# Optimization experiments

Measured on AMD Instinct MI355X. Metric: run time of the kernel, lower is better.

## Reference

```python
import jax, jax.numpy as jnp
import numpy as np
from jax import lax

NBINS = 256


def setup_inputs() -> dict:
    key = jax.random.key(0)
    y_pred = jax.random.uniform(key, (64, 3, 512, 512), dtype=jnp.float32)
    return {"y_pred": y_pred}


def reference(y_pred):
    # Faithful to: per-batch torch.histc(bins=256) (range = data min/max),
    # normalize to probs, entropy in bits with 0*log2(0)=0, mean over batch.
    B = y_pred.shape[0]
    x = y_pred.reshape(B, -1)  # [B, N]
    mn = jnp.min(x, axis=1, keepdims=True)
    mx = jnp.max(x, axis=1, keepdims=True)
    # torch.histc: if min == max they are adjusted to min-1 / max+1
    rng = jnp.where(mx > mn, mx - mn, 2.0)
    lo = jnp.where(mx > mn, mn, mn - 1.0)
    idx = jnp.clip(((x - lo) * (NBINS / rng)).astype(jnp.int32), 0, NBINS - 1)
    idx = lax.stop_gradient(idx)  # binning is non-differentiable (as in torch.histc)
    hist = jax.vmap(lambda i: jnp.bincount(i, length=NBINS))(idx)  # [B, 256]
    hist = hist.astype(y_pred.dtype)
    p = hist / jnp.sum(hist, axis=1, keepdims=True)
    safe_p = jnp.where(p == 0, 1.0, p)  # log2(1)=0 -> contributes 0
    ent = -jnp.sum(p * jnp.log2(safe_p), axis=1)  # [B], entropy in bits
    return jnp.mean(ent)
```

## Files before the change

kernel.cpp:

```cpp
#include <hip/hip_runtime.h>

#define NBINS   256
#define B       64
#define NPB     786432
#define NF4     (NPB / 4)
#define BPB1    32
#define BPB2    16
#define THREADS 256

__global__ __launch_bounds__(THREADS) void k_minmax(const float4* __restrict__ x,
                                                    float* __restrict__ pmn,
                                                    float* __restrict__ pmx) {
    const int batch = blockIdx.x / BPB1;
    const int blk   = blockIdx.x % BPB1;
    const float4* p = x + (long long)batch * NF4;

    float mn = 3.402823466e38f, mx = -3.402823466e38f;
    #pragma unroll 4
    for (int i = blk * THREADS + threadIdx.x; i < NF4; i += BPB1 * THREADS) {
        float4 v = p[i];
        mn = fminf(mn, fminf(fminf(v.x, v.y), fminf(v.z, v.w)));
        mx = fmaxf(mx, fmaxf(fmaxf(v.x, v.y), fmaxf(v.z, v.w)));
    }
    for (int o = 32; o > 0; o >>= 1) {
        mn = fminf(mn, __shfl_down(mn, o));
        mx = fmaxf(mx, __shfl_down(mx, o));
    }
    __shared__ float smn[4], smx[4];
    int wid = threadIdx.x >> 6;
    if ((threadIdx.x & 63) == 0) { smn[wid] = mn; smx[wid] = mx; }
    __syncthreads();
    if (threadIdx.x == 0) {
        pmn[blockIdx.x] = fminf(fminf(smn[0], smn[1]), fminf(smn[2], smn[3]));
        pmx[blockIdx.x] = fmaxf(fmaxf(smx[0], smx[1]), fmaxf(smx[2], smx[3]));
    }
}

__global__ __launch_bounds__(THREADS) void k_hist(const float4* __restrict__ x,
                                                  const float* __restrict__ pmn,
                                                  const float* __restrict__ pmx,
                                                  unsigned* __restrict__ part) {
    __shared__ unsigned lh[NBINS * 32];
    __shared__ float s_lo, s_scale;

    const int batch = blockIdx.x / BPB2;
    const int blk   = blockIdx.x % BPB2;

    for (int i = threadIdx.x; i < NBINS * 32; i += THREADS) lh[i] = 0u;

    if (threadIdx.x < 64) {
        int l = threadIdx.x & 31;
        float mn = pmn[batch * BPB1 + l];
        float mx = pmx[batch * BPB1 + l];
        for (int o = 16; o > 0; o >>= 1) {
            mn = fminf(mn, __shfl_down(mn, o));
            mx = fmaxf(mx, __shfl_down(mx, o));
        }
        if (threadIdx.x == 0) {
            float rng = (mx > mn) ? (mx - mn) : 2.0f;
            s_lo      = (mx > mn) ? mn : (mn - 1.0f);
            s_scale   = (float)NBINS / rng;
        }
    }
    __syncthreads();

    const float lo    = s_lo;
    const float scale = s_scale;
    const int   g     = threadIdx.x & 31;
    const float4* p   = x + (long long)batch * NF4;

    #pragma unroll 2
    for (int i = blk * THREADS + threadIdx.x; i < NF4; i += BPB2 * THREADS) {
        float4 v = p[i];
        int i0 = min(max((int)((v.x - lo) * scale), 0), NBINS - 1);
        int i1 = min(max((int)((v.y - lo) * scale), 0), NBINS - 1);
        int i2 = min(max((int)((v.z - lo) * scale), 0), NBINS - 1);
        int i3 = min(max((int)((v.w - lo) * scale), 0), NBINS - 1);
        atomicAdd(&lh[i0 * 32 + g], 1u);
        atomicAdd(&lh[i1 * 32 + g], 1u);
        atomicAdd(&lh[i2 * 32 + g], 1u);
        atomicAdd(&lh[i3 * 32 + g], 1u);
    }
    __syncthreads();

    unsigned s = 0;
    #pragma unroll
    for (int j = 0; j < 32; ++j)
        s += lh[threadIdx.x * 32 + ((j + threadIdx.x) & 31)];
    part[blockIdx.x * NBINS + threadIdx.x] = s;
}

__global__ __launch_bounds__(THREADS) void k_ent(const unsigned* __restrict__ part,
                                                 float* __restrict__ ent) {
    const int b = blockIdx.x;
    unsigned c = 0;
    #pragma unroll
    for (int j = 0; j < BPB2; ++j)
        c += part[(b * BPB2 + j) * NBINS + threadIdx.x];

    float s = 0.0f;
    if (c) {
        float pv = (float)c * (1.0f / (float)NPB);
        s = pv * log2f(pv);
    }
    for (int o = 32; o > 0; o >>= 1) s += __shfl_down(s, o);
    __shared__ float sw[4];
    int wid = threadIdx.x >> 6;
    if ((threadIdx.x & 63) == 0) sw[wid] = s;
    __syncthreads();
    if (threadIdx.x == 0)
        ent[b] = -(sw[0] + sw[1] + sw[2] + sw[3]);
}

__global__ __launch_bounds__(64) void k_mean(const float* __restrict__ ent,
                                             float* __restrict__ out) {
    float v = ent[threadIdx.x];
    for (int o = 32; o > 0; o >>= 1) v += __shfl_down(v, o);
    if (threadIdx.x == 0) out[0] = v * (1.0f / (float)B);
}

extern "C" void kernel_launch(void* const* d_in, const int* in_sizes, int n_in,
                              void* d_out, int out_size, void* d_ws, size_t ws_size,
                              hipStream_t stream) {
    const float* x = (const float*)d_in[0];
    float* out = (float*)d_out;

    float*    pmn  = (float*)d_ws;
    float*    pmx  = pmn + B * BPB1;
    unsigned* part = (unsigned*)(pmx + B * BPB1);
    float*    ent  = (float*)(part + B * BPB2 * NBINS);

    hipLaunchKernelGGL(k_minmax, dim3(B * BPB1), dim3(THREADS), 0, stream,
                       (const float4*)x, pmn, pmx);
    hipLaunchKernelGGL(k_hist, dim3(B * BPB2), dim3(THREADS), 0, stream,
                       (const float4*)x, pmn, pmx, part);
    hipLaunchKernelGGL(k_ent, dim3(B), dim3(THREADS), 0, stream, part, ent);
    hipLaunchKernelGGL(k_mean, dim3(1), dim3(64), 0, stream, ent, out);
}
```

Measured before the change: 303.3 us.

## Double hist block size, dual-accumulate minmax, fuse mean into entropy kernel

Min/max reduction now uses a fixed 12-iteration loop with two independent accumulators to raise memory-level parallelism. The histogram kernel runs 512 threads per block for more in-flight loads, at the cost of more lanes sharing each privatized sub-histogram. The separate mean kernel is removed: the entropy kernel uses an atomic counter, reset in the minmax kernel, so the last block computes the batch mean. This saves a launch but adds fences and an atomic.

Result: no change. 304.6 us (+0.4%).

```diff
diff --git a/kernel.cpp b/kernel.cpp
--- a/kernel.cpp
+++ b/kernel.cpp
@@ -6,22 +6,33 @@
 #define NF4     (NPB / 4)
 #define BPB1    32
 #define BPB2    16
-#define THREADS 256
+#define T1      256
+#define T2      512
 
-__global__ __launch_bounds__(THREADS) void k_minmax(const float4* __restrict__ x,
-                                                    float* __restrict__ pmn,
-                                                    float* __restrict__ pmx) {
+__global__ __launch_bounds__(T1) void k_minmax(const float4* __restrict__ x,
+                                               float* __restrict__ pmn,
+                                               float* __restrict__ pmx,
+                                               unsigned* __restrict__ counter) {
+    if (blockIdx.x == 0 && threadIdx.x == 0) counter[0] = 0u;
+
     const int batch = blockIdx.x / BPB1;
     const int blk   = blockIdx.x % BPB1;
     const float4* p = x + (long long)batch * NF4;
 
-    float mn = 3.402823466e38f, mx = -3.402823466e38f;
+    float mn0 = 3.402823466e38f, mx0 = -3.402823466e38f;
+    float mn1 = 3.402823466e38f, mx1 = -3.402823466e38f;
+    const int stride = BPB1 * T1;
+    int i = blk * T1 + threadIdx.x;
     #pragma unroll 4
-    for (int i = blk * THREADS + threadIdx.x; i < NF4; i += BPB1 * THREADS) {
-        float4 v = p[i];
-        mn = fminf(mn, fminf(fminf(v.x, v.y), fminf(v.z, v.w)));
-        mx = fmaxf(mx, fmaxf(fmaxf(v.x, v.y), fmaxf(v.z, v.w)));
+    for (int it = 0; it < 12; ++it, i += 2 * stride) {
+        float4 a = p[i];
+        float4 b = p[i + stride];
+        mn0 = fminf(mn0, fminf(fminf(a.x, a.y), fminf(a.z, a.w)));
+        mx0 = fmaxf(mx0, fmaxf(fmaxf(a.x, a.y), fmaxf(a.z, a.w)));
+        mn1 = fminf(mn1, fminf(fminf(b.x, b.y), fminf(b.z, b.w)));
+        mx1 = fmaxf(mx1, fmaxf(fmaxf(b.x, b.y), fmaxf(b.z, b.w)));
     }
+    float mn = fminf(mn0, mn1), mx = fmaxf(mx0, mx1);
     for (int o = 32; o > 0; o >>= 1) {
         mn = fminf(mn, __shfl_down(mn, o));
         mx = fmaxf(mx, __shfl_down(mx, o));
@@ -36,17 +47,17 @@
     }
 }
 
-__global__ __launch_bounds__(THREADS) void k_hist(const float4* __restrict__ x,
-                                                  const float* __restrict__ pmn,
-                                                  const float* __restrict__ pmx,
-                                                  unsigned* __restrict__ part) {
+__global__ __launch_bounds__(T2) void k_hist(const float4* __restrict__ x,
+                                             const float* __restrict__ pmn,
+                                             const float* __restrict__ pmx,
+                                             unsigned* __restrict__ part) {
     __shared__ unsigned lh[NBINS * 32];
     __shared__ float s_lo, s_scale;
 
     const int batch = blockIdx.x / BPB2;
     const int blk   = blockIdx.x % BPB2;
 
-    for (int i = threadIdx.x; i < NBINS * 32; i += THREADS) lh[i] = 0u;
+    for (int i = threadIdx.x; i < NBINS * 32; i += T2) lh[i] = 0u;
 
     if (threadIdx.x < 64) {
         int l = threadIdx.x & 31;
@@ -70,7 +81,7 @@
     const float4* p   = x + (long long)batch * NF4;
 
     #pragma unroll 2
-    for (int i = blk * THREADS + threadIdx.x; i < NF4; i += BPB2 * THREADS) {
+    for (int i = blk * T2 + threadIdx.x; i < NF4; i += BPB2 * T2) {
         float4 v = p[i];
         int i0 = min(max((int)((v.x - lo) * scale), 0), NBINS - 1);
         int i1 = min(max((int)((v.y - lo) * scale), 0), NBINS - 1);
@@ -83,15 +94,19 @@
     }
     __syncthreads();
 
-    unsigned s = 0;
-    #pragma unroll
-    for (int j = 0; j < 32; ++j)
-        s += lh[threadIdx.x * 32 + ((j + threadIdx.x) & 31)];
-    part[blockIdx.x * NBINS + threadIdx.x] = s;
+    if (threadIdx.x < NBINS) {
+        unsigned s = 0;
+        #pragma unroll
+        for (int j = 0; j < 32; ++j)
+            s += lh[threadIdx.x * 32 + ((j + threadIdx.x) & 31)];
+        part[blockIdx.x * NBINS + threadIdx.x] = s;
+    }
 }
 
-__global__ __launch_bounds__(THREADS) void k_ent(const unsigned* __restrict__ part,
-                                                 float* __restrict__ ent) {
+__global__ __launch_bounds__(T1) void k_ent(const unsigned* __restrict__ part,
+                                            float* __restrict__ ent,
+                                            unsigned* __restrict__ counter,
+                                            float* __restrict__ out) {
     const int b = blockIdx.x;
     unsigned c = 0;
     #pragma unroll
@@ -105,18 +120,25 @@
     }
     for (int o = 32; o > 0; o >>= 1) s += __shfl_down(s, o);
     __shared__ float sw[4];
+    __shared__ int last;
     int wid = threadIdx.x >> 6;
     if ((threadIdx.x & 63) == 0) sw[wid] = s;
     __syncthreads();
-    if (threadIdx.x == 0)
+    if (threadIdx.x == 0) {
         ent[b] = -(sw[0] + sw[1] + sw[2] + sw[3]);
-}
-
-__global__ __launch_bounds__(64) void k_mean(const float* __restrict__ ent,
-                                             float* __restrict__ out) {
-    float v = ent[threadIdx.x];
-    for (int o = 32; o > 0; o >>= 1) v += __shfl_down(v, o);
-    if (threadIdx.x == 0) out[0] = v * (1.0f / (float)B);
+        __threadfence();
+        unsigned old = atomicAdd(counter, 1u);
+        last = (old == B - 1) ? 1 : 0;
+    }
+    __syncthreads();
+    if (last) {
+        __threadfence();
+        if (threadIdx.x < 64) {
+            float v = ent[threadIdx.x];
+            for (int o = 32; o > 0; o >>= 1) v += __shfl_down(v, o);
+            if (threadIdx.x == 0) out[0] = v * (1.0f / (float)B);
+        }
+    }
 }
 
 extern "C" void kernel_launch(void* const* d_in, const int* in_sizes, int n_in,
@@ -129,11 +151,11 @@
     float*    pmx  = pmn + B * BPB1;
     unsigned* part = (unsigned*)(pmx + B * BPB1);
     float*    ent  = (float*)(part + B * BPB2 * NBINS);
+    unsigned* cnt  = (unsigned*)(ent + B);
 
-    hipLaunchKernelGGL(k_minmax, dim3(B * BPB1), dim3(THREADS), 0, stream,
-                       (const float4*)x, pmn, pmx);
-    hipLaunchKernelGGL(k_hist, dim3(B * BPB2), dim3(THREADS), 0, stream,
+    hipLaunchKernelGGL(k_minmax, dim3(B * BPB1), dim3(T1), 0, stream,
+                       (const float4*)x, pmn, pmx, cnt);
+    hipLaunchKernelGGL(k_hist, dim3(B * BPB2), dim3(T2), 0, stream,
                        (const float4*)x, pmn, pmx, part);
-    hipLaunchKernelGGL(k_ent, dim3(B), dim3(THREADS), 0, stream, part, ent);
-    hipLaunchKernelGGL(k_mean, dim3(1), dim3(64), 0, stream, ent, out);
+    hipLaunchKernelGGL(k_ent, dim3(B), dim3(T1), 0, stream, part, ent, cnt, out);
 }
```
